# Kernel optimization log

Measured on AMD Instinct MI355X. Metric: run time of the kernel, lower is better.

## Reference

```python
import jax, jax.numpy as jnp
import numpy as np

MARGIN = 0.1
PERM_SEED = 42  # fixed stand-in for torch.randperm per row


def setup_inputs() -> dict:
    key = jax.random.key(0)
    k1, k2, k3 = jax.random.split(key, 3)
    n, d, f = 32768, 1000, 300
    inputs = jax.random.normal(k1, (n, f), dtype=jnp.float32)
    Y = jax.random.normal(k2, (d, f), dtype=jnp.float32)
    y_idxs = jax.random.randint(k3, (n,), 0, d)
    return {"inputs": inputs, "Y": Y, "y_idxs": y_idxs}


def reference(inputs, Y, y_idxs):
    # inputs: [n, f], Y: [d, f] class semantic embeddings, y_idxs: [n]
    n, d = inputs.shape[0], Y.shape[0]

    # All dot products at once: S[i, j] = Y[j] . inputs[i]
    S = inputs @ Y.T  # [n, d]

    # One random class permutation per row (torch.randperm(d) per sample)
    perm_keys = jax.random.split(jax.random.key(PERM_SEED), n)
    perms = jax.vmap(lambda k: jax.random.permutation(k, d))(perm_keys)  # [n, d]

    ap = S[jnp.arange(n), y_idxs]                 # [n]   anchor-positive dots
    an = jnp.take_along_axis(S, perms, axis=1)    # [n, d] anchor-negative dots in perm order

    valid = perms != y_idxs[:, None]              # skip j == y
    # early-break condition at each permutation slot
    cond = valid & ((ap[:, None] - an) > MARGIN)
    c = cond.astype(jnp.int32)
    excl_cum = jnp.cumsum(c, axis=1) - c          # exclusive cumsum of break events
    # include every valid slot up to AND including the first breaking slot
    include = valid & (excl_cum == 0)             # [n, d]

    # MarginRankingLoss with target=1: mean(max(0, margin + an - ap))
    per_pair = jnp.maximum(0.0, MARGIN + an - ap[:, None])
    total = jnp.sum(jnp.where(include, per_pair, 0.0))
    count = jnp.maximum(jnp.sum(include), 1).astype(jnp.float32)
    return total / count
```

## Files before the change

kernel.cpp:

```cpp
#include <hip/hip_runtime.h>
#include <stdint.h>

#define N_ROWS 32768
#define D_CLS  1000
#define D_PAD  1024
#define F_DIM  300
#define F_PAD  320
#define MARGIN 0.1f

#define M_PB   32
#define NTHR   512
#define NT_PW  8
#define MT_PB  2
#define LDA    328
#define SROW   34

#define NPART  32

typedef short short8 __attribute__((ext_vector_type(8)));
typedef float f32x4  __attribute__((ext_vector_type(4)));

__device__ __forceinline__ uint32_t rotl32(uint32_t x, int r) {
  return (x << r) | (x >> (32 - r));
}

__device__ __forceinline__ void threefry2x32(uint32_t k0, uint32_t k1,
                                             uint32_t x0, uint32_t x1,
                                             uint32_t& o0, uint32_t& o1) {
  uint32_t k2 = k0 ^ k1 ^ 0x1BD11BDAu;
  x0 += k0; x1 += k1;
#define TF_R(r) { x0 += x1; x1 = rotl32(x1, (r)); x1 ^= x0; }
  TF_R(13) TF_R(15) TF_R(26) TF_R(6)
  x0 += k1; x1 += k2 + 1u;
  TF_R(17) TF_R(29) TF_R(16) TF_R(24)
  x0 += k2; x1 += k0 + 2u;
  TF_R(13) TF_R(15) TF_R(26) TF_R(6)
  x0 += k0; x1 += k1 + 3u;
  TF_R(17) TF_R(29) TF_R(16) TF_R(24)
  x0 += k1; x1 += k2 + 4u;
  TF_R(13) TF_R(15) TF_R(26) TF_R(6)
  x0 += k2; x1 += k0 + 5u;
#undef TF_R
  o0 = x0; o1 = x1;
}

struct TFSched {
  uint32_t k0, k1, k2, k2p1, k0p2, k1p3, k2p4, k0p5;
};
__device__ __forceinline__ TFSched tf_make(uint32_t k0, uint32_t k1) {
  TFSched s;
  s.k0 = k0; s.k1 = k1;
  s.k2 = k0 ^ k1 ^ 0x1BD11BDAu;
  s.k2p1 = s.k2 + 1u; s.k0p2 = k0 + 2u; s.k1p3 = k1 + 3u;
  s.k2p4 = s.k2 + 4u; s.k0p5 = k0 + 5u;
  return s;
}
__device__ __forceinline__ uint32_t tf_hash(const TFSched& s, uint32_t c) {
  uint32_t x0 = s.k0, x1 = c + s.k1;
#define TFH(r) { x0 += x1; x1 = __builtin_amdgcn_alignbit(x1, x1, 32 - (r)); x1 ^= x0; }
  TFH(13) TFH(15) TFH(26) TFH(6)
  x0 += s.k1; x1 += s.k2p1;
  TFH(17) TFH(29) TFH(16) TFH(24)
  x0 += s.k2; x1 += s.k0p2;
  TFH(13) TFH(15) TFH(26) TFH(6)
  x0 += s.k0; x1 += s.k1p3;
  TFH(17) TFH(29) TFH(16) TFH(24)
  x0 += s.k1; x1 += s.k2p4;
  TFH(13) TFH(15) TFH(26) TFH(6)
  x0 += s.k2; x1 += s.k0p5;
#undef TFH
  return x0 ^ x1;
}

__device__ __forceinline__ uint16_t f2bf(float f) {
  uint32_t u = __builtin_bit_cast(uint32_t, f);
  return (uint16_t)((u + 0x7FFFu + ((u >> 16) & 1u)) >> 16);
}
__device__ __forceinline__ float bf2f(uint16_t v) {
  return __builtin_bit_cast(float, (uint32_t)v << 16);
}

__global__ void prep(const float* __restrict__ Y, uint16_t* __restrict__ Ybf) {
  int i = blockIdx.x * 256 + threadIdx.x;
  if (i < D_PAD * F_PAD) {
    int j = i / F_PAD;
    int k = i - j * F_PAD;
    float v = (j < D_CLS && k < F_DIM) ? Y[j * F_DIM + k] : 0.f;
    Ybf[i] = f2bf(v);
  }
}

__launch_bounds__(NTHR, 4)
__global__ void triplet_fused(const float* __restrict__ inputs,
                              const uint16_t* __restrict__ Ybf,
                              const int* __restrict__ yidx,
                              float* __restrict__ rowSum,
                              int* __restrict__ rowCnt) {
  __shared__ __align__(16) uint16_t SH[D_PAD * SROW];
  __shared__ int      y_sh[M_PB];
  __shared__ uint32_t subk_sh[M_PB][2];

  const int t    = threadIdx.x;
  const int wave = t >> 6;
  const int lane = t & 63;
  const int l15  = lane & 15;
  const int g    = lane >> 4;
  const int row0 = blockIdx.x * M_PB;
  const int colbase = wave * (NT_PW * 16);

  if (t < M_PB) {
    y_sh[t] = yidx[row0 + t];
    uint32_t r1, r2, s1, s2;
    threefry2x32(0u, 42u, 0u, (uint32_t)(row0 + t), r1, r2);
    threefry2x32(r1, r2, 0u, 1u, s1, s2);
    subk_sh[t][0] = s1; subk_sh[t][1] = s2;
  }

  uint16_t* A_fl = SH;
  for (int i = t; i < M_PB * (F_DIM / 4); i += NTHR) {
    int r  = i / 75;
    int c4 = i - r * 75;
    float4 v = *(const float4*)(inputs + (size_t)(row0 + r) * F_DIM + c4 * 4);
    ushort4 o;
    o.x = f2bf(v.x); o.y = f2bf(v.y); o.z = f2bf(v.z); o.w = f2bf(v.w);
    *(ushort4*)&A_fl[r * LDA + c4 * 4] = o;
  }
  for (int i = t; i < M_PB * 5; i += NTHR) {
    int r = i / 5, p = i - r * 5;
    *(ushort4*)&A_fl[r * LDA + 300 + p * 4] = (ushort4){0, 0, 0, 0};
  }
  __syncthreads();

  f32x4 acc[MT_PB][NT_PW];
#pragma unroll
  for (int mt = 0; mt < MT_PB; ++mt)
#pragma unroll
    for (int nt = 0; nt < NT_PW; ++nt) acc[mt][nt] = (f32x4){0.f, 0.f, 0.f, 0.f};

  const uint16_t* gB[NT_PW];
#pragma unroll
  for (int nt = 0; nt < NT_PW; ++nt) {
    int j = colbase + nt * 16 + l15;
    gB[nt] = Ybf + (size_t)j * F_PAD + (g << 3);
  }
  const uint16_t* aBase = &A_fl[l15 * LDA + (g << 3)];

#pragma unroll 2
  for (int ks = 0; ks < F_PAD / 32; ++ks) {
    short8 b[NT_PW], a[MT_PB];
#pragma unroll
    for (int nt = 0; nt < NT_PW; ++nt)
      b[nt] = *(const short8*)(gB[nt] + ks * 32);
#pragma unroll
    for (int mt = 0; mt < MT_PB; ++mt)
      a[mt] = *(const short8*)(aBase + mt * 16 * LDA + ks * 32);
#pragma unroll
    for (int mt = 0; mt < MT_PB; ++mt)
#pragma unroll
      for (int nt = 0; nt < NT_PW; ++nt)
        acc[mt][nt] = __builtin_amdgcn_mfma_f32_16x16x32_bf16(a[mt], b[nt], acc[mt][nt], 0, 0, 0);
  }

  __syncthreads();

#pragma unroll
  for (int mt = 0; mt < MT_PB; ++mt)
#pragma unroll
    for (int nt = 0; nt < NT_PW; ++nt) {
      int col = colbase + nt * 16 + l15;
#pragma unroll
      for (int p = 0; p < 2; ++p) {
        uint32_t lo = f2bf(acc[mt][nt][2 * p]);
        uint32_t hi = f2bf(acc[mt][nt][2 * p + 1]);
        *(uint32_t*)&SH[col * SROW + mt * 16 + (g << 2) + 2 * p] = (hi << 16) | lo;
      }
    }
  __syncthreads();

#pragma unroll 1
  for (int pr = 0; pr < 2; ++pr) {
    const int rA = wave * 4 + pr * 2;
    const int rB = rA + 1;
    const int yA = y_sh[rA], yB = y_sh[rB];
    const TFSched sA = tf_make(subk_sh[rA][0], subk_sh[rA][1]);
    const TFSched sB = tf_make(subk_sh[rB][0], subk_sh[rB][1]);
    const float apA = bf2f(SH[yA * SROW + rA]);
    const float apB = bf2f(SH[yB * SROW + rB]);

    uint32_t skAB[16];
    uint32_t pkA = 0xFFFFFFFFu, pkB = 0xFFFFFFFFu;
#pragma unroll
    for (int q = 0; q < 16; ++q) {
      const int c = q * 64 + lane;
      uint32_t kA = tf_hash(sA, (uint32_t)c);
      uint32_t kB = tf_hash(sB, (uint32_t)c);
      skAB[q] = (kA >> 16) | (kB & 0xFFFF0000u);
      float anA = bf2f(SH[c * SROW + rA]);
      float anB = bf2f(SH[c * SROW + rB]);
      if ((c < D_CLS) && (c != yA) && (apA - anA) > MARGIN) {
        pkA = (kA < pkA) ? kA : pkA;
      }
      if ((c < D_CLS) && (c != yB) && (apB - anB) > MARGIN) {
        pkB = (kB < pkB) ? kB : pkB;
      }
    }
#pragma unroll
    for (int off = 1; off < 64; off <<= 1) {
      uint32_t oA = __shfl_xor(pkA, off, 64);
      uint32_t oB = __shfl_xor(pkB, off, 64);
      pkA = (oA < pkA) ? oA : pkA;
      pkB = (oB < pkB) ? oB : pkB;
    }
    const uint32_t pA16 = pkA >> 16;
    const uint32_t pB16 = pkB >> 16;

    float smA = 0.f, smB = 0.f; int ctA = 0, ctB = 0;
#pragma unroll
    for (int q = 0; q < 16; ++q) {
      const int c = q * 64 + lane;
      float anA = bf2f(SH[c * SROW + rA]);
      float anB = bf2f(SH[c * SROW + rB]);
      if ((c < D_CLS) && (c != yA) && (skAB[q] & 0xFFFFu) < pA16) {
        smA += MARGIN + anA - apA; ctA += 1;
      }
      if ((c < D_CLS) && (c != yB) && (skAB[q] >> 16) < pB16) {
        smB += MARGIN + anB - apB; ctB += 1;
      }
    }
#pragma unroll
    for (int off = 1; off < 64; off <<= 1) {
      smA += __shfl_xor(smA, off, 64);
      smB += __shfl_xor(smB, off, 64);
      ctA += __shfl_xor(ctA, off, 64);
      ctB += __shfl_xor(ctB, off, 64);
    }
    if (lane == 0) {
      rowSum[row0 + rA] = smA;
      rowCnt[row0 + rA] = ctA + (pkA != 0xFFFFFFFFu ? 1 : 0);
      rowSum[row0 + rB] = smB;
      rowCnt[row0 + rB] = ctB + (pkB != 0xFFFFFFFFu ? 1 : 0);
    }
  }
}

__global__ void reduce_part(const float* __restrict__ rowSum,
                            const int* __restrict__ rowCnt,
                            float* __restrict__ pS, int* __restrict__ pC) {
  __shared__ float ss[4];
  __shared__ int   sc[4];
  const int base = blockIdx.x * (N_ROWS / NPART);
  float s = 0.f; int c = 0;
  for (int i = threadIdx.x; i < N_ROWS / NPART; i += 256) {
    s += rowSum[base + i];
    c += rowCnt[base + i];
  }
#pragma unroll
  for (int off = 32; off > 0; off >>= 1) {
    s += __shfl_down(s, (unsigned)off, 64);
    c += __shfl_down(c, (unsigned)off, 64);
  }
  int wid = threadIdx.x >> 6, lane = threadIdx.x & 63;
  if (lane == 0) { ss[wid] = s; sc[wid] = c; }
  __syncthreads();
  if (threadIdx.x == 0) {
    pS[blockIdx.x] = ss[0] + ss[1] + ss[2] + ss[3];
    pC[blockIdx.x] = sc[0] + sc[1] + sc[2] + sc[3];
  }
}

__global__ void reduce_final(const float* __restrict__ pS,
                             const int* __restrict__ pC,
                             float* __restrict__ out) {
  const int lane = threadIdx.x;
  float s = (lane < NPART) ? pS[lane] : 0.f;
  int   c = (lane < NPART) ? pC[lane] : 0;
#pragma unroll
  for (int off = 32; off > 0; off >>= 1) {
    s += __shfl_down(s, (unsigned)off, 64);
    c += __shfl_down(c, (unsigned)off, 64);
  }
  if (lane == 0) out[0] = s / (float)(c < 1 ? 1 : c);
}

extern "C" void kernel_launch(void* const* d_in, const int* in_sizes, int n_in,
                              void* d_out, int out_size, void* d_ws, size_t ws_size,
                              hipStream_t stream) {
  const float* inputs = (const float*)d_in[0];
  const float* Y      = (const float*)d_in[1];
  const int*   yidx   = (const int*)d_in[2];
  float* out = (float*)d_out;

  char* ws = (char*)d_ws;
  size_t off = 0;
  uint16_t* Ybf    = (uint16_t*)(ws + off); off += (size_t)D_PAD * F_PAD * 2;
  float*    rowSum = (float*)(ws + off);    off += (size_t)N_ROWS * 4;
  int*      rowCnt = (int*)(ws + off);      off += (size_t)N_ROWS * 4;
  float*    pS     = (float*)(ws + off);    off += (size_t)NPART * 4;
  int*      pC     = (int*)(ws + off);      off += (size_t)NPART * 4;

  hipLaunchKernelGGL(prep, dim3((D_PAD * F_PAD + 255) / 256), dim3(256),
                     0, stream, Y, Ybf);
  hipLaunchKernelGGL(triplet_fused, dim3(N_ROWS / M_PB), dim3(NTHR),
                     0, stream, inputs, Ybf, yidx, rowSum, rowCnt);
  hipLaunchKernelGGL(reduce_part, dim3(NPART), dim3(256), 0, stream,
                     rowSum, rowCnt, pS, pC);
  hipLaunchKernelGGL(reduce_final, dim3(1), dim3(64), 0, stream, pS, pC, out);
}
```

Baseline: 151.6 us.

## Shrink fused block to 16 rows, overlap A staging with score buffer

The fused kernel now handles 16 rows per block instead of 32. Each wave computes two passes of 64 columns with 4 accumulators, and the bf16 A tile sits at the tail of the shared score buffer so the first pass's scores can be written before the second pass. The smaller LDS footprint and fewer registers allow 8 blocks per CU, and each wave handles one row pair, loading both rows' scores with a single 32-bit LDS read and using readfirstlane for uniform values. The cost is twice the blocks and twice the Y reads from global/L2 per row, plus an extra barrier phase.

```diff
diff --git a/kernel.cpp b/kernel.cpp
--- a/kernel.cpp
+++ b/kernel.cpp
@@ -8,12 +8,11 @@
 #define F_PAD  320
 #define MARGIN 0.1f
 
-#define M_PB   32
-#define NTHR   512
-#define NT_PW  8
-#define MT_PB  2
+#define M16    16
+#define F16THR 512
 #define LDA    328
-#define SROW   34
+#define SRW    18
+#define A_OFF  (D_PAD * SRW - M16 * LDA)
 
 #define NPART  32
 
@@ -79,6 +78,12 @@
 __device__ __forceinline__ float bf2f(uint16_t v) {
   return __builtin_bit_cast(float, (uint32_t)v << 16);
 }
+__device__ __forceinline__ float bf2f_lo(uint32_t v) {
+  return __builtin_bit_cast(float, v << 16);
+}
+__device__ __forceinline__ float bf2f_hi(uint32_t v) {
+  return __builtin_bit_cast(float, v & 0xFFFF0000u);
+}
 
 __global__ void prep(const float* __restrict__ Y, uint16_t* __restrict__ Ybf) {
   int i = blockIdx.x * 256 + threadIdx.x;
@@ -90,34 +95,33 @@
   }
 }
 
-__launch_bounds__(NTHR, 4)
-__global__ void triplet_fused(const float* __restrict__ inputs,
-                              const uint16_t* __restrict__ Ybf,
-                              const int* __restrict__ yidx,
-                              float* __restrict__ rowSum,
-                              int* __restrict__ rowCnt) {
-  __shared__ __align__(16) uint16_t SH[D_PAD * SROW];
-  __shared__ int      y_sh[M_PB];
-  __shared__ uint32_t subk_sh[M_PB][2];
+__launch_bounds__(F16THR, 8)
+__global__ void fused16(const float* __restrict__ inputs,
+                        const uint16_t* __restrict__ Ybf,
+                        const int* __restrict__ yidx,
+                        float* __restrict__ rowSum,
+                        int* __restrict__ rowCnt) {
+  __shared__ __align__(16) uint16_t SH[D_PAD * SRW];
+  __shared__ int      y_sh[M16];
+  __shared__ uint32_t sk_sh[M16][2];
 
   const int t    = threadIdx.x;
   const int wave = t >> 6;
   const int lane = t & 63;
   const int l15  = lane & 15;
   const int g    = lane >> 4;
-  const int row0 = blockIdx.x * M_PB;
-  const int colbase = wave * (NT_PW * 16);
-
-  if (t < M_PB) {
+  const int row0 = blockIdx.x * M16;
+
+  if (t < M16) {
     y_sh[t] = yidx[row0 + t];
     uint32_t r1, r2, s1, s2;
     threefry2x32(0u, 42u, 0u, (uint32_t)(row0 + t), r1, r2);
     threefry2x32(r1, r2, 0u, 1u, s1, s2);
-    subk_sh[t][0] = s1; subk_sh[t][1] = s2;
-  }
-
-  uint16_t* A_fl = SH;
-  for (int i = t; i < M_PB * (F_DIM / 4); i += NTHR) {
+    sk_sh[t][0] = s1; sk_sh[t][1] = s2;
+  }
+
+  uint16_t* A_fl = SH + A_OFF;
+  for (int i = t; i < M16 * (F_DIM / 4); i += F16THR) {
     int r  = i / 75;
     int c4 = i - r * 75;
     float4 v = *(const float4*)(inputs + (size_t)(row0 + r) * F_DIM + c4 * 4);
@@ -125,67 +129,87 @@
     o.x = f2bf(v.x); o.y = f2bf(v.y); o.z = f2bf(v.z); o.w = f2bf(v.w);
     *(ushort4*)&A_fl[r * LDA + c4 * 4] = o;
   }
-  for (int i = t; i < M_PB * 5; i += NTHR) {
-    int r = i / 5, p = i - r * 5;
+  for (int i = t; i < M16 * 7; i += F16THR) {
+    int r = i / 7, p = i - r * 7;
     *(ushort4*)&A_fl[r * LDA + 300 + p * 4] = (ushort4){0, 0, 0, 0};
   }
   __syncthreads();
 
-  f32x4 acc[MT_PB][NT_PW];
-#pragma unroll
-  for (int mt = 0; mt < MT_PB; ++mt)
-#pragma unroll
-    for (int nt = 0; nt < NT_PW; ++nt) acc[mt][nt] = (f32x4){0.f, 0.f, 0.f, 0.f};
-
-  const uint16_t* gB[NT_PW];
-#pragma unroll
-  for (int nt = 0; nt < NT_PW; ++nt) {
-    int j = colbase + nt * 16 + l15;
-    gB[nt] = Ybf + (size_t)j * F_PAD + (g << 3);
-  }
-  const uint16_t* aBase = &A_fl[l15 * LDA + (g << 3)];
-
+  const uint16_t* aBase = A_fl + l15 * LDA + g * 8;
+
+  {
+    f32x4 acc[4];
+#pragma unroll
+    for (int nt = 0; nt < 4; ++nt) acc[nt] = (f32x4){0.f, 0.f, 0.f, 0.f};
+    const uint16_t* gBp = Ybf + (size_t)(wave * 64 + l15) * F_PAD + g * 8;
 #pragma unroll 2
-  for (int ks = 0; ks < F_PAD / 32; ++ks) {
-    short8 b[NT_PW], a[MT_PB];
-#pragma unroll
-    for (int nt = 0; nt < NT_PW; ++nt)
-      b[nt] = *(const short8*)(gB[nt] + ks * 32);
-#pragma unroll
-    for (int mt = 0; mt < MT_PB; ++mt)
-      a[mt] = *(const short8*)(aBase + mt * 16 * LDA + ks * 32);
-#pragma unroll
-    for (int mt = 0; mt < MT_PB; ++mt)
-#pragma unroll
-      for (int nt = 0; nt < NT_PW; ++nt)
-        acc[mt][nt] = __builtin_amdgcn_mfma_f32_16x16x32_bf16(a[mt], b[nt], acc[mt][nt], 0, 0, 0);
-  }
-
+    for (int ks = 0; ks < F_PAD / 32; ++ks) {
+      short8 b[4], a;
+#pragma unroll
+      for (int nt = 0; nt < 4; ++nt)
+        b[nt] = *(const short8*)(gBp + (size_t)nt * 16 * F_PAD + ks * 32);
+      a = *(const short8*)(aBase + ks * 32);
+#pragma unroll
+      for (int nt = 0; nt < 4; ++nt)
+        acc[nt] = __builtin_amdgcn_mfma_f32_16x16x32_bf16(a, b[nt], acc[nt], 0, 0, 0);
+    }
+#pragma unroll
+    for (int nt = 0; nt < 4; ++nt) {
+      const int col = wave * 64 + nt * 16 + l15;
+#pragma unroll
+      for (int p = 0; p < 2; ++p) {
+        uint32_t lo = f2bf(acc[nt][2 * p]);
+        uint32_t hi = f2bf(acc[nt][2 * p + 1]);
+        *(uint32_t*)&SH[col * SRW + g * 4 + 2 * p] = (hi << 16) | lo;
+      }
+    }
+  }
+
+  f32x4 acc1[4];
+#pragma unroll
+  for (int nt = 0; nt < 4; ++nt) acc1[nt] = (f32x4){0.f, 0.f, 0.f, 0.f};
+  {
+    const uint16_t* gBp = Ybf + (size_t)(512 + wave * 64 + l15) * F_PAD + g * 8;
+#pragma unroll 2
+    for (int ks = 0; ks < F_PAD / 32; ++ks) {
+      short8 b[4], a;
+#pragma unroll
+      for (int nt = 0; nt < 4; ++nt)
+        b[nt] = *(const short8*)(gBp + (size_t)nt * 16 * F_PAD + ks * 32);
+      a = *(const short8*)(aBase + ks * 32);
+#pragma unroll
+      for (int nt = 0; nt < 4; ++nt)
+        acc1[nt] = __builtin_amdgcn_mfma_f32_16x16x32_bf16(a, b[nt], acc1[nt], 0, 0, 0);
+    }
+  }
   __syncthreads();
 
 #pragma unroll
-  for (int mt = 0; mt < MT_PB; ++mt)
-#pragma unroll
-    for (int nt = 0; nt < NT_PW; ++nt) {
-      int col = colbase + nt * 16 + l15;
-#pragma unroll
-      for (int p = 0; p < 2; ++p) {
-        uint32_t lo = f2bf(acc[mt][nt][2 * p]);
-        uint32_t hi = f2bf(acc[mt][nt][2 * p + 1]);
-        *(uint32_t*)&SH[col * SROW + mt * 16 + (g << 2) + 2 * p] = (hi << 16) | lo;
-      }
-    }
+  for (int nt = 0; nt < 4; ++nt) {
+    const int col = 512 + wave * 64 + nt * 16 + l15;
+#pragma unroll
+    for (int p = 0; p < 2; ++p) {
+      uint32_t lo = f2bf(acc1[nt][2 * p]);
+      uint32_t hi = f2bf(acc1[nt][2 * p + 1]);
+      *(uint32_t*)&SH[col * SRW + g * 4 + 2 * p] = (hi << 16) | lo;
+    }
+  }
   __syncthreads();
 
-#pragma unroll 1
-  for (int pr = 0; pr < 2; ++pr) {
-    const int rA = wave * 4 + pr * 2;
-    const int rB = rA + 1;
-    const int yA = y_sh[rA], yB = y_sh[rB];
-    const TFSched sA = tf_make(subk_sh[rA][0], subk_sh[rA][1]);
-    const TFSched sB = tf_make(subk_sh[rB][0], subk_sh[rB][1]);
-    const float apA = bf2f(SH[yA * SROW + rA]);
-    const float apB = bf2f(SH[yB * SROW + rB]);
+  {
+    const int rA = row0 + 2 * wave;
+    const int yA = __builtin_amdgcn_readfirstlane(y_sh[2 * wave]);
+    const int yB = __builtin_amdgcn_readfirstlane(y_sh[2 * wave + 1]);
+    const uint32_t a1 = __builtin_amdgcn_readfirstlane(sk_sh[2 * wave][0]);
+    const uint32_t a2 = __builtin_amdgcn_readfirstlane(sk_sh[2 * wave][1]);
+    const uint32_t b1 = __builtin_amdgcn_readfirstlane(sk_sh[2 * wave + 1][0]);
+    const uint32_t b2 = __builtin_amdgcn_readfirstlane(sk_sh[2 * wave + 1][1]);
+    const TFSched sA = tf_make(a1, a2);
+    const TFSched sB = tf_make(b1, b2);
+    const float apA = bf2f((uint16_t)__builtin_amdgcn_readfirstlane(
+        (uint32_t)SH[yA * SRW + 2 * wave]));
+    const float apB = bf2f((uint16_t)__builtin_amdgcn_readfirstlane(
+        (uint32_t)SH[yB * SRW + 2 * wave + 1]));
 
     uint32_t skAB[16];
     uint32_t pkA = 0xFFFFFFFFu, pkB = 0xFFFFFFFFu;
@@ -195,8 +219,9 @@
       uint32_t kA = tf_hash(sA, (uint32_t)c);
       uint32_t kB = tf_hash(sB, (uint32_t)c);
       skAB[q] = (kA >> 16) | (kB & 0xFFFF0000u);
-      float anA = bf2f(SH[c * SROW + rA]);
-      float anB = bf2f(SH[c * SROW + rB]);
+      const uint32_t s32 = *(const uint32_t*)&SH[c * SRW + 2 * wave];
+      const float anA = bf2f_lo(s32);
+      const float anB = bf2f_hi(s32);
       if ((c < D_CLS) && (c != yA) && (apA - anA) > MARGIN) {
         pkA = (kA < pkA) ? kA : pkA;
       }
@@ -218,8 +243,9 @@
 #pragma unroll
     for (int q = 0; q < 16; ++q) {
       const int c = q * 64 + lane;
-      float anA = bf2f(SH[c * SROW + rA]);
-      float anB = bf2f(SH[c * SROW + rB]);
+      const uint32_t s32 = *(const uint32_t*)&SH[c * SRW + 2 * wave];
+      const float anA = bf2f_lo(s32);
+      const float anB = bf2f_hi(s32);
       if ((c < D_CLS) && (c != yA) && (skAB[q] & 0xFFFFu) < pA16) {
         smA += MARGIN + anA - apA; ctA += 1;
       }
@@ -235,10 +261,10 @@
       ctB += __shfl_xor(ctB, off, 64);
     }
     if (lane == 0) {
-      rowSum[row0 + rA] = smA;
-      rowCnt[row0 + rA] = ctA + (pkA != 0xFFFFFFFFu ? 1 : 0);
-      rowSum[row0 + rB] = smB;
-      rowCnt[row0 + rB] = ctB + (pkB != 0xFFFFFFFFu ? 1 : 0);
+      rowSum[rA]     = smA;
+      rowCnt[rA]     = ctA + (pkA != 0xFFFFFFFFu ? 1 : 0);
+      rowSum[rA + 1] = smB;
+      rowCnt[rA + 1] = ctB + (pkB != 0xFFFFFFFFu ? 1 : 0);
     }
   }
 }
@@ -300,7 +326,7 @@
 
   hipLaunchKernelGGL(prep, dim3((D_PAD * F_PAD + 255) / 256), dim3(256),
                      0, stream, Y, Ybf);
-  hipLaunchKernelGGL(triplet_fused, dim3(N_ROWS / M_PB), dim3(NTHR),
+  hipLaunchKernelGGL(fused16, dim3(N_ROWS / M16), dim3(F16THR),
                      0, stream, inputs, Ybf, yidx, rowSum, rowCnt);
   hipLaunchKernelGGL(reduce_part, dim3(NPART), dim3(256), 0, stream,
                      rowSum, rowCnt, pS, pC);
```

Measured after the change: 193.0 us. 1.27x slower.
